# Kernel tuning notes

Hardware: AMD Instinct MI355X
Metric: run time of the kernel (lower is better)

Reference implementation:

```python
import jax, jax.numpy as jnp
import numpy as np

N_NODES = 50000
N_EDGES = 800000
IN_DIM = 16
HID = 16
EDGE_DIM = 8
GRAPH_DIM = 8
OUT_DIM = 1
N_LAYERS = 3


def setup_inputs() -> dict:
    key = jax.random.key(0)
    ks = jax.random.split(key, 12)
    x = jax.random.normal(ks[0], (N_NODES, IN_DIM), dtype=jnp.float32)
    edge_index = jax.random.randint(ks[1], (2, N_EDGES), 0, N_NODES, dtype=jnp.int32)
    edge_attr = jax.random.normal(ks[2], (N_EDGES, EDGE_DIM), dtype=jnp.float32)
    graph_features = jax.random.normal(ks[3], (GRAPH_DIM, N_NODES), dtype=jnp.float32)
    # stacked per-layer params (all layers have in=hidden=16)
    nnW = jax.random.normal(ks[4], (N_LAYERS, EDGE_DIM, IN_DIM * HID), dtype=jnp.float32) * 0.1
    nnb = jax.random.normal(ks[5], (N_LAYERS, IN_DIM * HID), dtype=jnp.float32) * 0.1
    rootW = jax.random.normal(ks[6], (N_LAYERS, IN_DIM, HID), dtype=jnp.float32) * 0.1
    bias = jax.random.normal(ks[7], (N_LAYERS, HID), dtype=jnp.float32) * 0.1
    head_W = jax.random.normal(ks[8], (HID + GRAPH_DIM, OUT_DIM), dtype=jnp.float32) * 0.1
    head_b = jax.random.normal(ks[9], (OUT_DIM,), dtype=jnp.float32) * 0.1
    return {"x": x, "edge_index": edge_index, "edge_attr": edge_attr,
            "graph_features": graph_features, "nnW": nnW, "nnb": nnb,
            "rootW": rootW, "bias": bias, "head_W": head_W, "head_b": head_b}


def _nnconv(x, src, dst, edge_attr, nnW, nnb, rootW, bias):
    # edge MLP -> per-edge weight matrix [E, in, out]
    theta = (edge_attr @ nnW + nnb).reshape(-1, x.shape[1], rootW.shape[1])
    # per-edge matmul with gathered source features, scatter-add to targets
    msg = jnp.einsum('ei,eio->eo', x[src], theta)  # [E, out]
    agg = jax.ops.segment_sum(msg, dst, num_segments=N_NODES)
    return agg + x @ rootW + bias


def reference(x, edge_index, edge_attr, graph_features, nnW, nnb, rootW, bias, head_W, head_b):
    src, dst = edge_index[0], edge_index[1]
    for i in range(N_LAYERS):
        x = _nnconv(x, src, dst, edge_attr, nnW[i], nnb[i], rootW[i], bias[i])
        x = jax.nn.relu(x)
        # dropout p=0.0 / eval mode -> identity
    h = jnp.concatenate([x, graph_features.T], axis=1)  # [N, hid+graph_dim]
    return h @ head_W + head_b
```

## Files before the change

### kernel.cpp

```cpp
#include <hip/hip_runtime.h>
#include <hip/hip_fp16.h>

#define N_NODES 50000
#define N_EDGES 800000
#define IN_DIM 16
#define HID 16
#define EDGE_DIM 8
#define GRAPH_DIM 8
#define N_LAYERS 3
#define SCAN_BS 256
#define SCAN_NB ((N_NODES + SCAN_BS - 1) / SCAN_BS)

typedef unsigned uint4v __attribute__((ext_vector_type(4)));

__device__ __forceinline__ unsigned pack_h2(float lo, float hi) {
    __half2 h = __floats2half2_rn(lo, hi);
    return *reinterpret_cast<unsigned*>(&h);
}
__device__ __forceinline__ float2 unpack_h2(unsigned u) {
    __half2 h = *reinterpret_cast<__half2*>(&u);
    return __half22float2(h);
}

__global__ __launch_bounds__(256)
void hist_kernel(const int* __restrict__ ei, int* __restrict__ deg) {
    int e = blockIdx.x * blockDim.x + threadIdx.x;
    if (e < N_EDGES) atomicAdd(&deg[ei[N_EDGES + e]], 1);
}

__global__ __launch_bounds__(SCAN_BS)
void scan1_kernel(const int* __restrict__ deg, int* __restrict__ offs,
                  int* __restrict__ bsum) {
    __shared__ int s[SCAN_BS];
    int tid = threadIdx.x;
    int i = blockIdx.x * SCAN_BS + tid;
    int v = (i < N_NODES) ? deg[i] : 0;
    s[tid] = v;
    __syncthreads();
    for (int off = 1; off < SCAN_BS; off <<= 1) {
        int t = (tid >= off) ? s[tid - off] : 0;
        __syncthreads();
        s[tid] += t;
        __syncthreads();
    }
    if (i < N_NODES) offs[i] = s[tid] - v;
    if (tid == SCAN_BS - 1) bsum[blockIdx.x] = s[tid];
}

__global__ __launch_bounds__(SCAN_BS)
void scan2_kernel(int* __restrict__ bsum) {
    __shared__ int s[SCAN_BS];
    int tid = threadIdx.x;
    int v = (tid < SCAN_NB) ? bsum[tid] : 0;
    s[tid] = v;
    __syncthreads();
    for (int off = 1; off < SCAN_BS; off <<= 1) {
        int t = (tid >= off) ? s[tid - off] : 0;
        __syncthreads();
        s[tid] += t;
        __syncthreads();
    }
    if (tid < SCAN_NB) bsum[tid] = s[tid] - v;
}

__global__ __launch_bounds__(SCAN_BS)
void scan3_kernel(int* __restrict__ offs, const int* __restrict__ bsum,
                  int* __restrict__ cur) {
    int i = blockIdx.x * SCAN_BS + threadIdx.x;
    if (i < N_NODES) {
        int o = offs[i] + bsum[blockIdx.x];
        offs[i] = o;
        cur[i] = o;
    }
    if (i == 0) offs[N_NODES] = N_EDGES;
}

__global__ __launch_bounds__(256)
void fill_kernel(const int* __restrict__ ei, const float* __restrict__ ea,
                 int* __restrict__ cur, int* __restrict__ csr_src,
                 uint4v* __restrict__ ea_h) {
    int e = blockIdx.x * blockDim.x + threadIdx.x;
    if (e >= N_EDGES) return;
    int src = ei[e];
    int dst = ei[N_EDGES + e];
    const float4* eap = (const float4*)(ea + (size_t)e * EDGE_DIM);
    float4 e0 = eap[0];
    float4 e1 = eap[1];
    uint4v rec;
    rec.x = pack_h2(e0.x, e0.y);
    rec.y = pack_h2(e0.z, e0.w);
    rec.z = pack_h2(e1.x, e1.y);
    rec.w = pack_h2(e1.z, e1.w);
    int j = atomicAdd(&cur[dst], 1);
    csr_src[j] = src;
    ea_h[j] = rec;
}

__global__ __launch_bounds__(256)
void prep_kernel(const float* __restrict__ x_in,
                 const float* __restrict__ nnW,
                 const float* __restrict__ nnb,
                 const float* __restrict__ rootW,
                 const float* __restrict__ bias,
                 unsigned* __restrict__ zw_h,
                 float* __restrict__ rb,
                 int apply_relu) {
    int t = blockIdx.x * blockDim.x + threadIdx.x;
    if (t >= N_NODES * HID) return;
    int n = t >> 4;
    int o = t & 15;

    float xv[IN_DIM];
    const float* xr = x_in + n * IN_DIM;
#pragma unroll
    for (int i = 0; i < IN_DIM; ++i) {
        float v = xr[i];
        xv[i] = apply_relu ? fmaxf(v, 0.0f) : v;
    }

    float zk[EDGE_DIM];
#pragma unroll
    for (int k = 0; k < EDGE_DIM; ++k) zk[k] = 0.0f;
    float wv = 0.0f;
    float rv = bias[o];

#pragma unroll
    for (int i = 0; i < IN_DIM; ++i) {
        float xi = xv[i];
#pragma unroll
        for (int k = 0; k < EDGE_DIM; ++k) {
            zk[k] = fmaf(xi, nnW[k * 256 + i * 16 + o], zk[k]);
        }
        wv = fmaf(xi, nnb[i * 16 + o], wv);
        rv = fmaf(xi, rootW[i * 16 + o], rv);
    }

    unsigned* zn = zw_h + (size_t)n * 80;
#pragma unroll
    for (int kp = 0; kp < 4; ++kp) zn[kp * 16 + o] = pack_h2(zk[2 * kp], zk[2 * kp + 1]);
    zn[64 + o] = pack_h2(wv, 0.0f);
    rb[n * 16 + o] = rv;
}

__device__ __forceinline__ void edge_accum(const unsigned* __restrict__ zp,
                                           uint4v rec, int o, float& acc) {
    unsigned q0 = zp[o];
    unsigned q1 = zp[16 + o];
    unsigned q2 = zp[32 + o];
    unsigned q3 = zp[48 + o];
    unsigned q4 = zp[64 + o];
    float2 e01 = unpack_h2(rec.x);
    float2 e23 = unpack_h2(rec.y);
    float2 e45 = unpack_h2(rec.z);
    float2 e67 = unpack_h2(rec.w);
    float2 z01 = unpack_h2(q0);
    float2 z23 = unpack_h2(q1);
    float2 z45 = unpack_h2(q2);
    float2 z67 = unpack_h2(q3);
    float2 w_  = unpack_h2(q4);
    acc += w_.x;
    acc = fmaf(e01.x, z01.x, acc);
    acc = fmaf(e01.y, z01.y, acc);
    acc = fmaf(e23.x, z23.x, acc);
    acc = fmaf(e23.y, z23.y, acc);
    acc = fmaf(e45.x, z45.x, acc);
    acc = fmaf(e45.y, z45.y, acc);
    acc = fmaf(e67.x, z67.x, acc);
    acc = fmaf(e67.y, z67.y, acc);
}

template <bool DO_HEAD>
__global__ __launch_bounds__(256)
void agg_kernel(const int* __restrict__ offs,
                const int* __restrict__ csr_src,
                const uint4v* __restrict__ ea_h,
                const unsigned* __restrict__ zw_h,
                float* __restrict__ buf,
                const float* __restrict__ gf,
                const float* __restrict__ hW,
                const float* __restrict__ hb,
                float* __restrict__ out) {
    int tid = threadIdx.x;
    int o = tid & 15;
    int n = blockIdx.x * 16 + (tid >> 4);
    if (n >= N_NODES) return;

    float acc0 = buf[n * HID + o];
    float acc1 = 0.0f;
    int jb = offs[n], je = offs[n + 1];
    int j = jb;
    for (; j + 1 < je; j += 2) {
        int s0 = csr_src[j];
        int s1 = csr_src[j + 1];
        uint4v r0 = ea_h[j];
        uint4v r1 = ea_h[j + 1];
        const unsigned* zp0 = zw_h + (size_t)s0 * 80;
        const unsigned* zp1 = zw_h + (size_t)s1 * 80;
        edge_accum(zp0, r0, o, acc0);
        edge_accum(zp1, r1, o, acc1);
    }
    if (j < je) {
        int s0 = csr_src[j];
        uint4v r0 = ea_h[j];
        edge_accum(zw_h + (size_t)s0 * 80, r0, o, acc0);
    }
    float acc = acc0 + acc1;

    if (!DO_HEAD) {
        buf[n * HID + o] = acc;
    } else {
        float h = fmaxf(acc, 0.0f) * hW[o];
        if (o < GRAPH_DIM) h = fmaf(gf[o * N_NODES + n], hW[HID + o], h);
#pragma unroll
        for (int off = 8; off > 0; off >>= 1) h += __shfl_xor(h, off, 16);
        if (o == 0) out[n] = h + hb[0];
    }
}

extern "C" void kernel_launch(void* const* d_in, const int* in_sizes, int n_in,
                              void* d_out, int out_size, void* d_ws, size_t ws_size,
                              hipStream_t stream) {
    const float* x     = (const float*)d_in[0];
    const int*   ei    = (const int*)d_in[1];
    const float* ea    = (const float*)d_in[2];
    const float* gf    = (const float*)d_in[3];
    const float* nnW   = (const float*)d_in[4];
    const float* nnb   = (const float*)d_in[5];
    const float* rootW = (const float*)d_in[6];
    const float* bias  = (const float*)d_in[7];
    const float* hW    = (const float*)d_in[8];
    const float* hb    = (const float*)d_in[9];
    float* out = (float*)d_out;

    unsigned* zw_h = (unsigned*)d_ws;
    uint4v* ea_h   = (uint4v*)(zw_h + (size_t)N_NODES * 80);
    float* bufA    = (float*)(ea_h + N_EDGES);
    float* bufB    = bufA + (size_t)N_NODES * HID;
    int* csr_src   = (int*)(bufB + (size_t)N_NODES * HID);
    int* deg       = csr_src + N_EDGES;
    int* offs      = deg + N_NODES;
    int* cur       = offs + N_NODES + 8;
    int* bsum      = cur + N_NODES;

    dim3 blk(256);
    dim3 grid_e((N_EDGES + 255) / 256);
    dim3 grid_no((N_NODES * HID + 255) / 256);
    dim3 grid_a((N_NODES + 15) / 16);

    hipMemsetAsync(deg, 0, N_NODES * sizeof(int), stream);
    hist_kernel<<<grid_e, blk, 0, stream>>>(ei, deg);
    scan1_kernel<<<SCAN_NB, SCAN_BS, 0, stream>>>(deg, offs, bsum);
    scan2_kernel<<<1, SCAN_BS, 0, stream>>>(bsum);
    scan3_kernel<<<SCAN_NB, SCAN_BS, 0, stream>>>(offs, bsum, cur);
    fill_kernel<<<grid_e, blk, 0, stream>>>(ei, ea, cur, csr_src, ea_h);

    const float* xin = x;
    float* bufs[2] = {bufA, bufB};
    for (int l = 0; l < N_LAYERS; ++l) {
        float* buf = bufs[l & 1];
        prep_kernel<<<grid_no, blk, 0, stream>>>(
            xin,
            nnW + (size_t)l * EDGE_DIM * (IN_DIM * HID),
            nnb + (size_t)l * (IN_DIM * HID),
            rootW + (size_t)l * IN_DIM * HID,
            bias + (size_t)l * HID,
            zw_h, buf, l > 0 ? 1 : 0);
        if (l < N_LAYERS - 1) {
            agg_kernel<false><<<grid_a, blk, 0, stream>>>(
                offs, csr_src, ea_h, zw_h, buf, nullptr, nullptr, nullptr, nullptr);
        } else {
            agg_kernel<true><<<grid_a, blk, 0, stream>>>(
                offs, csr_src, ea_h, zw_h, buf, gf, hW, hb, out);
        }
        xin = buf;
    }
}
```

Measured before the change: 374.4 us.

## Fuse histogram with first prep, single-block scan, interleave CSR src with edge attrs

Merges the degree histogram and the layer-0 prep into one launch. Replaces the three-kernel scan with a single 1024-thread block scan that also writes the fill cursors. Packs each CSR record as a 24-byte struct holding the half-precision edge attributes and the source index, so the aggregation loop reads one record instead of two separate arrays. This cuts launches and separate loads, but a 24-byte stride is not 16-byte aligned, which may split vector loads, and a single-block scan serialises a small amount of work.

```diff
diff --git a/kernel.cpp b/kernel.cpp
--- a/kernel.cpp
+++ b/kernel.cpp
@@ -8,10 +8,14 @@
 #define EDGE_DIM 8
 #define GRAPH_DIM 8
 #define N_LAYERS 3
-#define SCAN_BS 256
-#define SCAN_NB ((N_NODES + SCAN_BS - 1) / SCAN_BS)
+#define HIST_BLOCKS ((N_EDGES + 255) / 256)
+#define PREP_BLOCKS ((N_NODES * HID + 255) / 256)
+#define SCAN_T 1024
+#define SCAN_CH ((N_NODES + SCAN_T - 1) / SCAN_T)
 
 typedef unsigned uint4v __attribute__((ext_vector_type(4)));
+
+struct Rec { unsigned e0, e1, e2, e3; int src; int pad; };
 
 __device__ __forceinline__ unsigned pack_h2(float lo, float hi) {
     __half2 h = __floats2half2_rn(lo, hi);
@@ -22,63 +26,99 @@
     return __half22float2(h);
 }
 
-__global__ __launch_bounds__(256)
-void hist_kernel(const int* __restrict__ ei, int* __restrict__ deg) {
-    int e = blockIdx.x * blockDim.x + threadIdx.x;
-    if (e < N_EDGES) atomicAdd(&deg[ei[N_EDGES + e]], 1);
-}
-
-__global__ __launch_bounds__(SCAN_BS)
-void scan1_kernel(const int* __restrict__ deg, int* __restrict__ offs,
-                  int* __restrict__ bsum) {
-    __shared__ int s[SCAN_BS];
+__device__ __forceinline__ void prep_one(int t, const float* __restrict__ x_in,
+                                         const float* __restrict__ nnW,
+                                         const float* __restrict__ nnb,
+                                         const float* __restrict__ rootW,
+                                         const float* __restrict__ bias,
+                                         unsigned* __restrict__ zw_h,
+                                         float* __restrict__ rb, int apply_relu) {
+    int n = t >> 4;
+    int o = t & 15;
+
+    float xv[IN_DIM];
+    const float* xr = x_in + n * IN_DIM;
+#pragma unroll
+    for (int i = 0; i < IN_DIM; ++i) {
+        float v = xr[i];
+        xv[i] = apply_relu ? fmaxf(v, 0.0f) : v;
+    }
+
+    float zk[EDGE_DIM];
+#pragma unroll
+    for (int k = 0; k < EDGE_DIM; ++k) zk[k] = 0.0f;
+    float wv = 0.0f;
+    float rv = bias[o];
+
+#pragma unroll
+    for (int i = 0; i < IN_DIM; ++i) {
+        float xi = xv[i];
+#pragma unroll
+        for (int k = 0; k < EDGE_DIM; ++k) {
+            zk[k] = fmaf(xi, nnW[k * 256 + i * 16 + o], zk[k]);
+        }
+        wv = fmaf(xi, nnb[i * 16 + o], wv);
+        rv = fmaf(xi, rootW[i * 16 + o], rv);
+    }
+
+    unsigned* zn = zw_h + (size_t)n * 80;
+#pragma unroll
+    for (int kp = 0; kp < 4; ++kp) zn[kp * 16 + o] = pack_h2(zk[2 * kp], zk[2 * kp + 1]);
+    zn[64 + o] = pack_h2(wv, 0.0f);
+    rb[n * 16 + o] = rv;
+}
+
+__global__ __launch_bounds__(256)
+void hist_prep0_kernel(const int* __restrict__ ei, int* __restrict__ deg,
+                       const float* __restrict__ x, const float* __restrict__ nnW,
+                       const float* __restrict__ nnb, const float* __restrict__ rootW,
+                       const float* __restrict__ bias,
+                       unsigned* __restrict__ zw_h, float* __restrict__ rb) {
+    if (blockIdx.x < HIST_BLOCKS) {
+        int e = blockIdx.x * 256 + threadIdx.x;
+        if (e < N_EDGES) atomicAdd(&deg[ei[N_EDGES + e]], 1);
+    } else {
+        int t = (blockIdx.x - HIST_BLOCKS) * 256 + threadIdx.x;
+        if (t < N_NODES * HID)
+            prep_one(t, x, nnW, nnb, rootW, bias, zw_h, rb, 0);
+    }
+}
+
+__global__ __launch_bounds__(SCAN_T)
+void scan_kernel(int* __restrict__ deg, int* __restrict__ offs) {
+    __shared__ int s[SCAN_T];
     int tid = threadIdx.x;
-    int i = blockIdx.x * SCAN_BS + tid;
-    int v = (i < N_NODES) ? deg[i] : 0;
-    s[tid] = v;
+    int base = tid * SCAN_CH;
+
+    int sum = 0;
+    for (int i = 0; i < SCAN_CH; ++i) {
+        int idx = base + i;
+        if (idx < N_NODES) sum += deg[idx];
+    }
+    s[tid] = sum;
     __syncthreads();
-    for (int off = 1; off < SCAN_BS; off <<= 1) {
+    for (int off = 1; off < SCAN_T; off <<= 1) {
         int t = (tid >= off) ? s[tid - off] : 0;
         __syncthreads();
         s[tid] += t;
         __syncthreads();
     }
-    if (i < N_NODES) offs[i] = s[tid] - v;
-    if (tid == SCAN_BS - 1) bsum[blockIdx.x] = s[tid];
-}
-
-__global__ __launch_bounds__(SCAN_BS)
-void scan2_kernel(int* __restrict__ bsum) {
-    __shared__ int s[SCAN_BS];
-    int tid = threadIdx.x;
-    int v = (tid < SCAN_NB) ? bsum[tid] : 0;
-    s[tid] = v;
-    __syncthreads();
-    for (int off = 1; off < SCAN_BS; off <<= 1) {
-        int t = (tid >= off) ? s[tid - off] : 0;
-        __syncthreads();
-        s[tid] += t;
-        __syncthreads();
-    }
-    if (tid < SCAN_NB) bsum[tid] = s[tid] - v;
-}
-
-__global__ __launch_bounds__(SCAN_BS)
-void scan3_kernel(int* __restrict__ offs, const int* __restrict__ bsum,
-                  int* __restrict__ cur) {
-    int i = blockIdx.x * SCAN_BS + threadIdx.x;
-    if (i < N_NODES) {
-        int o = offs[i] + bsum[blockIdx.x];
-        offs[i] = o;
-        cur[i] = o;
-    }
-    if (i == 0) offs[N_NODES] = N_EDGES;
+    int run = s[tid] - sum;
+    for (int i = 0; i < SCAN_CH; ++i) {
+        int idx = base + i;
+        if (idx < N_NODES) {
+            int d = deg[idx];
+            offs[idx] = run;
+            deg[idx] = run;
+            run += d;
+        }
+    }
+    if (tid == 0) offs[N_NODES] = N_EDGES;
 }
 
 __global__ __launch_bounds__(256)
 void fill_kernel(const int* __restrict__ ei, const float* __restrict__ ea,
-                 int* __restrict__ cur, int* __restrict__ csr_src,
-                 uint4v* __restrict__ ea_h) {
+                 int* __restrict__ cur, Rec* __restrict__ csr) {
     int e = blockIdx.x * blockDim.x + threadIdx.x;
     if (e >= N_EDGES) return;
     int src = ei[e];
@@ -86,60 +126,25 @@
     const float4* eap = (const float4*)(ea + (size_t)e * EDGE_DIM);
     float4 e0 = eap[0];
     float4 e1 = eap[1];
-    uint4v rec;
-    rec.x = pack_h2(e0.x, e0.y);
-    rec.y = pack_h2(e0.z, e0.w);
-    rec.z = pack_h2(e1.x, e1.y);
-    rec.w = pack_h2(e1.z, e1.w);
+    Rec r;
+    r.e0 = pack_h2(e0.x, e0.y);
+    r.e1 = pack_h2(e0.z, e0.w);
+    r.e2 = pack_h2(e1.x, e1.y);
+    r.e3 = pack_h2(e1.z, e1.w);
+    r.src = src;
+    r.pad = 0;
     int j = atomicAdd(&cur[dst], 1);
-    csr_src[j] = src;
-    ea_h[j] = rec;
-}
-
-__global__ __launch_bounds__(256)
-void prep_kernel(const float* __restrict__ x_in,
-                 const float* __restrict__ nnW,
-                 const float* __restrict__ nnb,
-                 const float* __restrict__ rootW,
+    csr[j] = r;
+}
+
+__global__ __launch_bounds__(256)
+void prep_kernel(const float* __restrict__ x_in, const float* __restrict__ nnW,
+                 const float* __restrict__ nnb, const float* __restrict__ rootW,
                  const float* __restrict__ bias,
-                 unsigned* __restrict__ zw_h,
-                 float* __restrict__ rb,
-                 int apply_relu) {
+                 unsigned* __restrict__ zw_h, float* __restrict__ rb) {
     int t = blockIdx.x * blockDim.x + threadIdx.x;
-    if (t >= N_NODES * HID) return;
-    int n = t >> 4;
-    int o = t & 15;
-
-    float xv[IN_DIM];
-    const float* xr = x_in + n * IN_DIM;
-#pragma unroll
-    for (int i = 0; i < IN_DIM; ++i) {
-        float v = xr[i];
-        xv[i] = apply_relu ? fmaxf(v, 0.0f) : v;
-    }
-
-    float zk[EDGE_DIM];
-#pragma unroll
-    for (int k = 0; k < EDGE_DIM; ++k) zk[k] = 0.0f;
-    float wv = 0.0f;
-    float rv = bias[o];
-
-#pragma unroll
-    for (int i = 0; i < IN_DIM; ++i) {
-        float xi = xv[i];
-#pragma unroll
-        for (int k = 0; k < EDGE_DIM; ++k) {
-            zk[k] = fmaf(xi, nnW[k * 256 + i * 16 + o], zk[k]);
-        }
-        wv = fmaf(xi, nnb[i * 16 + o], wv);
-        rv = fmaf(xi, rootW[i * 16 + o], rv);
-    }
-
-    unsigned* zn = zw_h + (size_t)n * 80;
-#pragma unroll
-    for (int kp = 0; kp < 4; ++kp) zn[kp * 16 + o] = pack_h2(zk[2 * kp], zk[2 * kp + 1]);
-    zn[64 + o] = pack_h2(wv, 0.0f);
-    rb[n * 16 + o] = rv;
+    if (t < N_NODES * HID)
+        prep_one(t, x_in, nnW, nnb, rootW, bias, zw_h, rb, 1);
 }
 
 __device__ __forceinline__ void edge_accum(const unsigned* __restrict__ zp,
@@ -172,8 +177,7 @@
 template <bool DO_HEAD>
 __global__ __launch_bounds__(256)
 void agg_kernel(const int* __restrict__ offs,
-                const int* __restrict__ csr_src,
-                const uint4v* __restrict__ ea_h,
+                const Rec* __restrict__ csr,
                 const unsigned* __restrict__ zw_h,
                 float* __restrict__ buf,
                 const float* __restrict__ gf,
@@ -190,19 +194,17 @@
     int jb = offs[n], je = offs[n + 1];
     int j = jb;
     for (; j + 1 < je; j += 2) {
-        int s0 = csr_src[j];
-        int s1 = csr_src[j + 1];
-        uint4v r0 = ea_h[j];
-        uint4v r1 = ea_h[j + 1];
-        const unsigned* zp0 = zw_h + (size_t)s0 * 80;
-        const unsigned* zp1 = zw_h + (size_t)s1 * 80;
-        edge_accum(zp0, r0, o, acc0);
-        edge_accum(zp1, r1, o, acc1);
+        Rec r0 = csr[j];
+        Rec r1 = csr[j + 1];
+        uint4v a0 = {r0.e0, r0.e1, r0.e2, r0.e3};
+        uint4v a1 = {r1.e0, r1.e1, r1.e2, r1.e3};
+        edge_accum(zw_h + (size_t)r0.src * 80, a0, o, acc0);
+        edge_accum(zw_h + (size_t)r1.src * 80, a1, o, acc1);
     }
     if (j < je) {
-        int s0 = csr_src[j];
-        uint4v r0 = ea_h[j];
-        edge_accum(zw_h + (size_t)s0 * 80, r0, o, acc0);
+        Rec r0 = csr[j];
+        uint4v a0 = {r0.e0, r0.e1, r0.e2, r0.e3};
+        edge_accum(zw_h + (size_t)r0.src * 80, a0, o, acc0);
     }
     float acc = acc0 + acc1;
 
@@ -233,45 +235,32 @@
     float* out = (float*)d_out;
 
     unsigned* zw_h = (unsigned*)d_ws;
-    uint4v* ea_h   = (uint4v*)(zw_h + (size_t)N_NODES * 80);
-    float* bufA    = (float*)(ea_h + N_EDGES);
-    float* bufB    = bufA + (size_t)N_NODES * HID;
-    int* csr_src   = (int*)(bufB + (size_t)N_NODES * HID);
-    int* deg       = csr_src + N_EDGES;
-    int* offs      = deg + N_NODES;
-    int* cur       = offs + N_NODES + 8;
-    int* bsum      = cur + N_NODES;
+    Rec* csr   = (Rec*)(zw_h + (size_t)N_NODES * 80);
+    float* bufA = (float*)((char*)csr + (size_t)N_EDGES * sizeof(Rec));
+    float* bufB = bufA + (size_t)N_NODES * HID;
+    int* deg    = (int*)(bufB + (size_t)N_NODES * HID);
+    int* offs   = deg + N_NODES;
 
     dim3 blk(256);
-    dim3 grid_e((N_EDGES + 255) / 256);
-    dim3 grid_no((N_NODES * HID + 255) / 256);
+    dim3 grid_e(HIST_BLOCKS);
+    dim3 grid_hp(HIST_BLOCKS + PREP_BLOCKS);
+    dim3 grid_no(PREP_BLOCKS);
     dim3 grid_a((N_NODES + 15) / 16);
 
     hipMemsetAsync(deg, 0, N_NODES * sizeof(int), stream);
-    hist_kernel<<<grid_e, blk, 0, stream>>>(ei, deg);
-    scan1_kernel<<<SCAN_NB, SCAN_BS, 0, stream>>>(deg, offs, bsum);
-    scan2_kernel<<<1, SCAN_BS, 0, stream>>>(bsum);
-    scan3_kernel<<<SCAN_NB, SCAN_BS, 0, stream>>>(offs, bsum, cur);
-    fill_kernel<<<grid_e, blk, 0, stream>>>(ei, ea, cur, csr_src, ea_h);
-
-    const float* xin = x;
-    float* bufs[2] = {bufA, bufB};
-    for (int l = 0; l < N_LAYERS; ++l) {
-        float* buf = bufs[l & 1];
-        prep_kernel<<<grid_no, blk, 0, stream>>>(
-            xin,
-            nnW + (size_t)l * EDGE_DIM * (IN_DIM * HID),
-            nnb + (size_t)l * (IN_DIM * HID),
-            rootW + (size_t)l * IN_DIM * HID,
-            bias + (size_t)l * HID,
-            zw_h, buf, l > 0 ? 1 : 0);
-        if (l < N_LAYERS - 1) {
-            agg_kernel<false><<<grid_a, blk, 0, stream>>>(
-                offs, csr_src, ea_h, zw_h, buf, nullptr, nullptr, nullptr, nullptr);
-        } else {
-            agg_kernel<true><<<grid_a, blk, 0, stream>>>(
-                offs, csr_src, ea_h, zw_h, buf, gf, hW, hb, out);
-        }
-        xin = buf;
-    }
-}
+    hist_prep0_kernel<<<grid_hp, blk, 0, stream>>>(ei, deg, x, nnW, nnb, rootW, bias,
+                                                   zw_h, bufA);
+    scan_kernel<<<1, SCAN_T, 0, stream>>>(deg, offs);
+    fill_kernel<<<grid_e, blk, 0, stream>>>(ei, ea, deg, csr);
+
+    agg_kernel<false><<<grid_a, blk, 0, stream>>>(offs, csr, zw_h, bufA,
+                                                  nullptr, nullptr, nullptr, nullptr);
+    prep_kernel<<<grid_no, blk, 0, stream>>>(bufA, nnW + 2048, nnb + 256,
+                                             rootW + 256, bias + 16, zw_h, bufB);
+    agg_kernel<false><<<grid_a, blk, 0, stream>>>(offs, csr, zw_h, bufB,
+                                                  nullptr, nullptr, nullptr, nullptr);
+    prep_kernel<<<grid_no, blk, 0, stream>>>(bufB, nnW + 4096, nnb + 512,
+                                             rootW + 512, bias + 32, zw_h, bufA);
+    agg_kernel<true><<<grid_a, blk, 0, stream>>>(offs, csr, zw_h, bufA,
+                                                 gf, hW, hb, out);
+}
```

Result: slower. 484.2 us (+29.3%).
